# Performance work log

Measured on AMD Instinct MI355X. Metric: run time of the kernel, lower is better.

## Reference

```python
import jax, jax.numpy as jnp
import numpy as np

DIM = 256
NUM_HEADS = 8
HEAD_DIM = DIM // NUM_HEADS
CPB_HIDDEN = 512
B, N = 2, 2304
TABLE = 9025  # (2*48-1)**2


def _l2norm(t, eps=1e-12):
    # matches torch F.normalize(dim=-1): x / max(||x||, eps)
    n = jnp.sqrt(jnp.sum(t * t, axis=-1, keepdims=True))
    return t / jnp.maximum(n, eps)


def setup_inputs() -> dict:
    key = jax.random.key(0)
    ks = jax.random.split(key, 12)
    x = jax.random.normal(ks[0], (B, N, DIM), dtype=jnp.float32)
    relative_pos_index = jax.random.randint(ks[1], (N, N), 0, TABLE, dtype=jnp.int64)
    relative_coords_table = jax.random.uniform(ks[2], (TABLE, 2), dtype=jnp.float32) * 2.0 - 1.0
    seq_length_scale = jnp.ones((1,), dtype=jnp.float32) * jnp.log2(jnp.float32(N))
    padding_mask = jnp.zeros((B, N), dtype=jnp.int32)
    s = 0.02
    W_qkv = jax.random.normal(ks[3], (3 * DIM, DIM), dtype=jnp.float32) * s
    b_qkv = jnp.zeros((3 * DIM,), dtype=jnp.float32)
    # temperature init: log(exp(1/0.24) - 1) so softplus(temperature) = 1/0.24
    temperature = jnp.full((NUM_HEADS, 1, 1), float(np.log(np.expm1(1.0 / 0.24))), dtype=jnp.float32)
    query_embedding = jax.random.normal(ks[4], (NUM_HEADS, 1, HEAD_DIM), dtype=jnp.float32) * s
    W_proj = jax.random.normal(ks[5], (DIM, DIM), dtype=jnp.float32) * s
    b_proj = jnp.zeros((DIM,), dtype=jnp.float32)
    W_cpb1 = jax.random.normal(ks[6], (CPB_HIDDEN, 2), dtype=jnp.float32) * s
    b_cpb1 = jnp.zeros((CPB_HIDDEN,), dtype=jnp.float32)
    W_cpb2 = jax.random.normal(ks[7], (NUM_HEADS, CPB_HIDDEN), dtype=jnp.float32) * s
    b_cpb2 = jnp.zeros((NUM_HEADS,), dtype=jnp.float32)
    return {
        'x': x, 'relative_pos_index': relative_pos_index,
        'relative_coords_table': relative_coords_table,
        'seq_length_scale': seq_length_scale, 'padding_mask': padding_mask,
        'W_qkv': W_qkv, 'b_qkv': b_qkv, 'temperature': temperature,
        'query_embedding': query_embedding, 'W_proj': W_proj, 'b_proj': b_proj,
        'W_cpb1': W_cpb1, 'b_cpb1': b_cpb1, 'W_cpb2': W_cpb2, 'b_cpb2': b_cpb2,
    }


def reference(x, relative_pos_index, relative_coords_table, seq_length_scale,
              padding_mask, W_qkv, b_qkv, temperature, query_embedding,
              W_proj, b_proj, W_cpb1, b_cpb1, W_cpb2, b_cpb2):
    Bx, Nx, C = x.shape
    h, d = NUM_HEADS, HEAD_DIM
    # qkv projection -> (B, 3h, N, d); first h heads = q, then k, then v
    qkv = (jnp.einsum('bnc,oc->bno', x, W_qkv) + b_qkv)
    qkv = qkv.reshape(Bx, Nx, 3 * h, d).transpose(0, 2, 1, 3)
    q, k, v = qkv[:, :h], qkv[:, h:2 * h], qkv[:, 2 * h:]
    # CPB relative bias: (T,2) -> (T,h) -> (h,N,N) via gather
    hid = jax.nn.relu(relative_coords_table @ W_cpb1.T + b_cpb1)
    tab = hid @ W_cpb2.T + b_cpb2                    # (T, h)
    rel_bias = tab.T[:, relative_pos_index.reshape(-1)].reshape(h, Nx, Nx)
    # cosine-sim attention with learned query embedding + softplus temperature
    scale = jax.nn.softplus(temperature) * seq_length_scale[0]   # (h,1,1)
    qn = (_l2norm(q) + query_embedding) * scale                  # (B,h,N,d)
    kn = _l2norm(k)
    attn = jnp.einsum('bhnd,bhmd->bhnm', qn, kn) + rel_bias
    attn = jax.nn.softmax(attn, axis=-1)
    out = jnp.einsum('bhnm,bhmd->bhnd', attn, v)
    out = out.transpose(0, 2, 1, 3).reshape(Bx, Nx, C)
    out = out @ W_proj.T + b_proj
    return out
```

## Files before the change

### kernel.cpp

```cpp
#include <hip/hip_runtime.h>
#include <math.h>

#define DIMC 256
#define NHEADS 8
#define HDIM 32
#define CPBH 512
#define BB 2
#define NSEQ 2304
#define TAB 9025
#define TABP 9040
#define RTOT (BB*NHEADS*NSEQ)
#define SPLITS 4
#define MSP (NSEQ/SPLITS)
#define PBS 36
#define NCHUNK (NSEQ/32)
#define LOG2E 1.44269504088896340736f

#define IDXP_ELEMS    (NSEQ * NCHUNK * 16)
#define IDXP4_BLOCKS  (IDXP_ELEMS / 1024)
#define CPB_BLOCKS    ((TAB + 63) / 64)
#define QKV_BLOCKS    (12 * 72)

typedef unsigned short ushort;
typedef __attribute__((ext_vector_type(8))) short short8;
typedef __attribute__((ext_vector_type(4))) short short4v;
typedef __attribute__((ext_vector_type(4))) float f32x4;

#define MFMA16(a,b,c) __builtin_amdgcn_mfma_f32_16x16x32_bf16((a),(b),(c),0,0,0)

#define GL16(SRC, DST) __builtin_amdgcn_global_load_lds( \
    (const __attribute__((address_space(1))) void*)(SRC), \
    (__attribute__((address_space(3))) void*)(DST), 16, 0, 0)

__device__ __forceinline__ ushort f2bf(float x) {
  unsigned u = __float_as_uint(x);
  u += 0x7FFFu + ((u >> 16) & 1u);
  return (ushort)(u >> 16);
}
__device__ __forceinline__ float bf2f(ushort b) {
  return __uint_as_float(((unsigned)b) << 16);
}
__device__ __forceinline__ float fexp2(float x) {
#if defined(__has_builtin)
#if __has_builtin(__builtin_amdgcn_exp2f)
  return __builtin_amdgcn_exp2f(x);
#else
  return exp2f(x);
#endif
#else
  return exp2f(x);
#endif
}
__device__ __forceinline__ unsigned pack_trunc(float p0, float p1) {
  return __builtin_amdgcn_perm(__float_as_uint(p1), __float_as_uint(p0), 0x07060302u);
}
__device__ __forceinline__ void cvt8(const float* __restrict__ p, short8* hi, short8* lo) {
  float4 v0 = *(const float4*)p;
  float4 v1 = *(const float4*)(p + 4);
  float vv[8] = {v0.x, v0.y, v0.z, v0.w, v1.x, v1.y, v1.z, v1.w};
  short8 h, l;
#pragma unroll
  for (int i = 0; i < 8; ++i) {
    ushort hh = f2bf(vv[i]);
    h[i] = (short)hh;
    l[i] = (short)f2bf(vv[i] - bf2f(hh));
  }
  *hi = h; *lo = l;
}

__launch_bounds__(256)
__global__ void pack_kernel(const int* __restrict__ idx, unsigned* __restrict__ idxP) {
  int t4 = blockIdx.x * 256 + threadIdx.x;
  int grp = t4 >> 4;
  int ch = grp % NCHUNK;
  int n4 = grp / NCHUNK;
  int m = ch * 32 + (t4 & 15);
  unsigned o[4];
#pragma unroll
  for (int i = 0; i < 4; ++i) {
    unsigned lo = (unsigned)idx[(size_t)(n4 * 4 + i) * NSEQ + m];
    unsigned hi = (unsigned)idx[(size_t)(n4 * 4 + i) * NSEQ + m + 16];
    o[i] = lo | (hi << 16);
  }
  *(uint4*)&idxP[(size_t)t4 * 4] = *(const uint4*)o;
}

__launch_bounds__(256)
__global__ void pre_kernel(const float* __restrict__ x, const float* __restrict__ wq,
                           const float* __restrict__ tbl, const float* __restrict__ W1,
                           const float* __restrict__ b1, const float* __restrict__ W2,
                           const float* __restrict__ b2,
                           const float* __restrict__ bias, const float* __restrict__ temp,
                           const float* __restrict__ sls, const float* __restrict__ qe,
                           ushort* __restrict__ qhi, ushort* __restrict__ qlo,
                           ushort* __restrict__ khi, ushort* __restrict__ klo,
                           ushort* __restrict__ vT, ushort* __restrict__ tabBf) {
  __shared__ __align__(16) ushort smemu[33792];
  int blk = blockIdx.x;
  int tid = threadIdx.x;

  if (blk < CPB_BLOCKS) {
    float* smem = (float*)smemu;
    float* w1b = smem;
    float* w2t = smem + 2048;
    float* part = smem + 6144;
    for (int i = tid; i < CPBH; i += 256) {
      w1b[i * 4 + 0] = W1[2 * i];
      w1b[i * 4 + 1] = W1[2 * i + 1];
      w1b[i * 4 + 2] = b1[i];
      w1b[i * 4 + 3] = 0.f;
    }
    for (int i = tid; i < CPBH * NHEADS; i += 256)
      w2t[(i & (CPBH - 1)) * NHEADS + (i >> 9)] = W2[i];
    int tl = tid & 63, jc = tid >> 6;
    int t = blk * 64 + tl;
    bool valid = t < TAB;
    float c0 = 0.f, c1 = 0.f;
    if (valid) { c0 = tbl[2 * t]; c1 = tbl[2 * t + 1]; }
    __syncthreads();
    float acc[NHEADS];
#pragma unroll
    for (int h = 0; h < NHEADS; ++h) acc[h] = 0.f;
    for (int j = jc * 128; j < jc * 128 + 128; ++j) {
      float4 wv = *(const float4*)&w1b[j * 4];
      float hid = fmaxf(fmaf(c0, wv.x, fmaf(c1, wv.y, wv.z)), 0.f);
      float4 wa = *(const float4*)&w2t[j * NHEADS];
      float4 wb = *(const float4*)&w2t[j * NHEADS + 4];
      acc[0] = fmaf(hid, wa.x, acc[0]);
      acc[1] = fmaf(hid, wa.y, acc[1]);
      acc[2] = fmaf(hid, wa.z, acc[2]);
      acc[3] = fmaf(hid, wa.w, acc[3]);
      acc[4] = fmaf(hid, wb.x, acc[4]);
      acc[5] = fmaf(hid, wb.y, acc[5]);
      acc[6] = fmaf(hid, wb.z, acc[6]);
      acc[7] = fmaf(hid, wb.w, acc[7]);
    }
#pragma unroll
    for (int h = 0; h < NHEADS; ++h) part[((size_t)jc * 64 + tl) * NHEADS + h] = acc[h];
    __syncthreads();
    if (jc == 0 && valid) {
#pragma unroll
      for (int h = 0; h < NHEADS; ++h) {
        float s = b2[h];
#pragma unroll
        for (int p = 0; p < 4; ++p) s += part[((size_t)p * 64 + tl) * NHEADS + h];
        tabBf[h * TABP + t] = f2bf(s * LOG2E);
      }
    }
  } else {
    ushort* bsh = smemu;
    ushort* bsl = smemu + 64 * 264;
    float (*vbuf)[65] = (float(*)[65])smemu;
    int t = blk - CPB_BLOCKS;
    int n0 = (t % 12) * 64, m0 = (t / 12) * 64;
    int lane = tid & 63, w = tid >> 6;
    int g = lane >> 4, c = lane & 15;
    int mw = m0 + w * 16;
    const int K = DIMC;

    {
      int rr = tid >> 2, cq = (tid & 3) * 64;
#pragma unroll
      for (int j = 0; j < 64; j += 8) {
        short8 hh, ll;
        cvt8(&wq[(size_t)(n0 + rr) * K + cq + j], &hh, &ll);
        *(short8*)&bsh[rr * 264 + cq + j] = hh;
        *(short8*)&bsl[rr * 264 + cq + j] = ll;
      }
    }
    __syncthreads();

    f32x4 acc[4] = {{0,0,0,0},{0,0,0,0},{0,0,0,0},{0,0,0,0}};
#pragma unroll 2
    for (int k0 = 0; k0 < K; k0 += 32) {
      short8 ah, al;
      cvt8(&x[(size_t)(mw + c) * K + k0 + g * 8], &ah, &al);
#pragma unroll
      for (int nt = 0; nt < 4; ++nt) {
        int br = (nt * 16 + c) * 264 + k0 + g * 8;
        short8 bh = *(const short8*)&bsh[br];
        short8 bl = *(const short8*)&bsl[br];
        acc[nt] = MFMA16(ah, bh, acc[nt]);
        acc[nt] = MFMA16(al, bh, acc[nt]);
        acc[nt] = MFMA16(ah, bl, acc[nt]);
      }
    }
#pragma unroll
    for (int nt = 0; nt < 4; ++nt) {
      float bv = bias[n0 + nt * 16 + c];
#pragma unroll
      for (int r = 0; r < 4; ++r) acc[nt][r] += bv;
    }
    __syncthreads();

    int b = (m0 >= NSEQ) ? 1 : 0;
    int nb = m0 - b * NSEQ;
    int sect = n0 >> 8;
    int hloc = (n0 & 255) >> 5;

    if (sect < 2) {
#pragma unroll
      for (int H = 0; H < 2; ++H) {
        int head = hloc + H;
        float scale = (sect == 0) ? log1pf(expf(temp[head])) * sls[0] * LOG2E : 0.f;
#pragma unroll
        for (int r = 0; r < 4; ++r) {
          float ss = acc[2*H][r]*acc[2*H][r] + acc[2*H+1][r]*acc[2*H+1][r];
          ss += __shfl_xor(ss, 1);
          ss += __shfl_xor(ss, 2);
          ss += __shfl_xor(ss, 4);
          ss += __shfl_xor(ss, 8);
          float inv = 1.f / fmaxf(sqrtf(ss), 1e-12f);
#pragma unroll
          for (int half = 0; half < 2; ++half) {
            int d = half * 16 + c;
            float val = acc[2*H + half][r] * inv;
            if (sect == 0) val = (val + qe[head * HDIM + d]) * scale;
            vbuf[w * 16 + g * 4 + r][H * 32 + d] = val;
          }
        }
      }
      __syncthreads();
      int plane = tid >> 7;
      int seg = tid & 127;
      int head = seg >> 6, row = seg & 63;
      const float* srcrow = &vbuf[row][head * 32];
      ushort out16[32];
#pragma unroll
      for (int i = 0; i < 32; ++i) {
        float v = srcrow[i];
        ushort hh = f2bf(v);
        out16[i] = plane ? f2bf(v - bf2f(hh)) : hh;
      }
      ushort* dstp = plane ? (sect == 0 ? qlo : klo) : (sect == 0 ? qhi : khi);
      size_t off = ((size_t)(b * NHEADS + hloc + head) * NSEQ + nb + row) * HDIM;
#pragma unroll
      for (int q4 = 0; q4 < 4; ++q4)
        *(int4*)&dstp[off + q4 * 8] = ((int4*)out16)[q4];
    } else {
#pragma unroll
      for (int nt = 0; nt < 4; ++nt)
#pragma unroll
        for (int r = 0; r < 4; ++r)
          vbuf[w * 16 + g * 4 + r][nt * 16 + c] = acc[nt][r];
      __syncthreads();
      int hbase = (n0 - 512) >> 5;
#pragma unroll
      for (int it = 0; it < 16; ++it) {
        int dloc = (tid >> 6) * 16 + it;
        int p = tid & 63;
        int pp = p & 31;
        int nsrc = (p & 32) + (pp & 1) * 16 + (pp >> 1);
        float v = vbuf[nsrc][dloc];
        int head = hbase + (dloc >> 5), d = dloc & 31;
        vT[((size_t)((b * NHEADS + head) * HDIM + d)) * NSEQ + nb + p] = f2bf(v);
      }
    }
  }
}

__launch_bounds__(256)
__global__ void attn_kernel(const ushort* __restrict__ qhi, const ushort* __restrict__ qlo,
                            const ushort* __restrict__ khi, const ushort* __restrict__ klo,
                            const ushort* __restrict__ vT, const ushort* __restrict__ tabBf,
                            const unsigned* __restrict__ idxP,
                            float* __restrict__ pO, float* __restrict__ pL) {
  __shared__ ushort tbf[10240];
  __shared__ __align__(16) ushort pbuf[16][16 * PBS];
  __shared__ __align__(16) ushort stg[2][6144];
  int tid = threadIdx.x;
  int lane = tid & 63;
  int w = tid >> 6;

  int bid = blockIdx.x;
  int qb = bid >> 5;
  int k8 = bid & 7;
  int j4 = (bid >> 3) & 3;
  int y  = k8 + 8 * j4;
  int s = y & 3, h = y >> 2;

  const ushort* tsrc = tabBf + h * TABP;
#pragma unroll
  for (int i = 0; i < 5; ++i) {
    int off = i * 2048 + tid * 8;
    *(int4*)&tbf[off] = *(const int4*)&tsrc[off];
  }

  int g = lane >> 4, c = lane & 15;
  int q0 = qb * 128 + w * 32;
  int qg0 = q0 >> 2;
  size_t rowA = (size_t)h * NSEQ;
  size_t rowB = (size_t)(NHEADS + h) * NSEQ;
  int m0 = s * MSP;

  int su   = tid & 127;
  int srow = su & 31;
  int sslt = su >> 5;
  const ushort* kb0 = (tid < 128) ? khi : klo;
  const ushort* sA = kb0 + (rowA + m0 + srow) * HDIM + sslt * 8;
  const ushort* sB = kb0 + (rowB + m0 + srow) * HDIM + sslt * 8;
  const ushort* sV = vT + ((size_t)(((tid < 128) ? h : NHEADS + h) * HDIM + srow)) * NSEQ
                     + m0 + sslt * 8;
  unsigned dwb = (unsigned)(tid & 192) * 8;

#define STAGE(DP) do {                         \
    GL16(sA, (DP) + dwb);                      \
    GL16(sB, (DP) + 2048 + dwb);               \
    GL16(sV, (DP) + 4096 + dwb);               \
    sA += 32 * HDIM; sB += 32 * HDIM; sV += 32; \
  } while (0)

  short8 qA0h = *(const short8*)&qhi[(rowA + q0 + c) * HDIM + g * 8];
  short8 qA0l = *(const short8*)&qlo[(rowA + q0 + c) * HDIM + g * 8];
  short8 qA1h = *(const short8*)&qhi[(rowA + q0 + 16 + c) * HDIM + g * 8];
  short8 qA1l = *(const short8*)&qlo[(rowA + q0 + 16 + c) * HDIM + g * 8];
  short8 qB0h = *(const short8*)&qhi[(rowB + q0 + c) * HDIM + g * 8];
  short8 qB0l = *(const short8*)&qlo[(rowB + q0 + c) * HDIM + g * 8];
  short8 qB1h = *(const short8*)&qhi[(rowB + q0 + 16 + c) * HDIM + g * 8];
  short8 qB1l = *(const short8*)&qlo[(rowB + q0 + 16 + c) * HDIM + g * 8];

  const unsigned IOFF1 = 4u * NCHUNK * 64;
  unsigned oIb = (unsigned)(((unsigned)(qg0 + g) * NCHUNK + (m0 >> 5)) * 64 + c * 4);
  unsigned oI  = oIb;
  uint4 ia = *(const uint4*)&idxP[oI];
  uint4 ja = *(const uint4*)&idxP[oI + IOFF1];

  STAGE(&stg[0][0]);
  __syncthreads();

  short one = (c == 0) ? (short)0x3F80 : (short)0;
  short8 onesB = {one, one, one, one, one, one, one, one};

  f32x4 oa00 = {0,0,0,0}, oa01 = {0,0,0,0}, oa10 = {0,0,0,0}, oa11 = {0,0,0,0};
  f32x4 ob00 = {0,0,0,0}, ob01 = {0,0,0,0}, ob10 = {0,0,0,0}, ob11 = {0,0,0,0};
  f32x4 la0 = {0,0,0,0}, la1 = {0,0,0,0}, lb0 = {0,0,0,0}, lb1 = {0,0,0,0};
  ushort* pba0 = pbuf[w * 4];
  ushort* pba1 = pbuf[w * 4 + 1];
  ushort* pbb0 = pbuf[w * 4 + 2];
  ushort* pbb1 = pbuf[w * 4 + 3];

  int kbo = g * 256 + c * 8;
  int cur = 0;

  for (int mt = m0; mt < m0 + MSP; mt += 32) {
    bool lastit = (mt + 32 >= m0 + MSP);

    asm volatile("s_waitcnt vmcnt(0)" ::: "memory");
    __builtin_amdgcn_s_barrier();
    __builtin_amdgcn_sched_barrier(0);

    unsigned oIn = lastit ? oIb : oI + 64;
    uint4 ian = *(const uint4*)&idxP[oIn];
    uint4 jan = *(const uint4*)&idxP[oIn + IOFF1];
    oI = oIn;
    if (!lastit) STAGE(&stg[cur ^ 1][0]);

    const ushort* S = &stg[cur][0];
    short8 ak0h = *(const short8*)&S[kbo];
    short8 ak1h = *(const short8*)&S[kbo + 128];
    short8 ak0l = *(const short8*)&S[1024 + kbo];
    short8 ak1l = *(const short8*)&S[1024 + kbo + 128];
    short8 bk0h = *(const short8*)&S[2048 + kbo];
    short8 bk1h = *(const short8*)&S[2048 + kbo + 128];
    short8 bk0l = *(const short8*)&S[3072 + kbo];
    short8 bk1l = *(const short8*)&S[3072 + kbo + 128];

    f32x4 sa0 = {0,0,0,0}, sa1 = {0,0,0,0}, ta0 = {0,0,0,0}, ta1 = {0,0,0,0};
    f32x4 sb0 = {0,0,0,0}, sb1 = {0,0,0,0}, tb0 = {0,0,0,0}, tb1 = {0,0,0,0};
    sa0 = MFMA16(qA0h, ak0h, sa0);
    sa1 = MFMA16(qA0h, ak1h, sa1);
    ta0 = MFMA16(qA1h, ak0h, ta0);
    ta1 = MFMA16(qA1h, ak1h, ta1);
    sb0 = MFMA16(qB0h, bk0h, sb0);
    sb1 = MFMA16(qB0h, bk1h, sb1);
    tb0 = MFMA16(qB1h, bk0h, tb0);
    tb1 = MFMA16(qB1h, bk1h, tb1);
    sa0 = MFMA16(qA0l, ak0h, sa0);
    sa1 = MFMA16(qA0l, ak1h, sa1);
    ta0 = MFMA16(qA1l, ak0h, ta0);
    ta1 = MFMA16(qA1l, ak1h, ta1);
    sb0 = MFMA16(qB0l, bk0h, sb0);
    sb1 = MFMA16(qB0l, bk1h, sb1);
    tb0 = MFMA16(qB1l, bk0h, tb0);
    tb1 = MFMA16(qB1l, bk1h, tb1);
    sa0 = MFMA16(qA0h, ak0l, sa0);
    sa1 = MFMA16(qA0h, ak1l, sa1);
    ta0 = MFMA16(qA1h, ak0l, ta0);
    ta1 = MFMA16(qA1h, ak1l, ta1);
    sb0 = MFMA16(qB0h, bk0l, sb0);
    sb1 = MFMA16(qB0h, bk1l, sb1);
    tb0 = MFMA16(qB1h, bk0l, tb0);
    tb1 = MFMA16(qB1h, bk1l, tb1);

    unsigned ip[4] = {ia.x, ia.y, ia.z, ia.w};
    unsigned jp[4] = {ja.x, ja.y, ja.z, ja.w};
#pragma unroll
    for (int r = 0; r < 4; ++r) {
      float b0 = bf2f(tbf[ip[r] & 0xFFFF]);
      float b1 = bf2f(tbf[ip[r] >> 16]);
      *(unsigned*)&pba0[(g * 4 + r) * PBS + 2 * c] =
          pack_trunc(fexp2(sa0[r] + b0), fexp2(sa1[r] + b1));
      *(unsigned*)&pbb0[(g * 4 + r) * PBS + 2 * c] =
          pack_trunc(fexp2(sb0[r] + b0), fexp2(sb1[r] + b1));
      float d0 = bf2f(tbf[jp[r] & 0xFFFF]);
      float d1 = bf2f(tbf[jp[r] >> 16]);
      *(unsigned*)&pba1[(g * 4 + r) * PBS + 2 * c] =
          pack_trunc(fexp2(ta0[r] + d0), fexp2(ta1[r] + d1));
      *(unsigned*)&pbb1[(g * 4 + r) * PBS + 2 * c] =
          pack_trunc(fexp2(tb0[r] + d0), fexp2(tb1[r] + d1));
    }

#define LOADP(PB, DST) do {                                             \
    short4v pA_ = *(const short4v*)&(PB)[c * PBS + g * 8];              \
    short4v pB_ = *(const short4v*)&(PB)[c * PBS + g * 8 + 4];          \
    DST = __builtin_shufflevector(pA_, pB_, 0, 1, 2, 3, 4, 5, 6, 7);    \
  } while (0)
    short8 pfa0, pfa1, pfb0, pfb1;
    LOADP(pba0, pfa0);
    LOADP(pba1, pfa1);
    LOADP(pbb0, pfb0);
    LOADP(pbb1, pfb1);
#undef LOADP

    short8 vf0 = *(const short8*)&S[4096 + kbo];
    short8 vf1 = *(const short8*)&S[4096 + kbo + 128];
    short8 wf0 = *(const short8*)&S[5120 + kbo];
    short8 wf1 = *(const short8*)&S[5120 + kbo + 128];

    oa00 = MFMA16(pfa0, vf0, oa00);
    oa01 = MFMA16(pfa0, vf1, oa01);
    oa10 = MFMA16(pfa1, vf0, oa10);
    oa11 = MFMA16(pfa1, vf1, oa11);
    ob00 = MFMA16(pfb0, wf0, ob00);
    ob01 = MFMA16(pfb0, wf1, ob01);
    ob10 = MFMA16(pfb1, wf0, ob10);
    ob11 = MFMA16(pfb1, wf1, ob11);
    la0  = MFMA16(pfa0, onesB, la0);
    la1  = MFMA16(pfa1, onesB, la1);
    lb0  = MFMA16(pfb0, onesB, lb0);
    lb1  = MFMA16(pfb1, onesB, lb1);

    ia = ian; ja = jan;
    cur ^= 1;
  }
#undef STAGE

  asm volatile("s_waitcnt vmcnt(0)" ::: "memory");

  size_t prowA = (size_t)s * RTOT + rowA;
  size_t prowB = (size_t)s * RTOT + rowB;
#pragma unroll
  for (int r = 0; r < 4; ++r) {
    size_t pa0 = prowA + q0 + g * 4 + r;
    pO[pa0 * HDIM + c]      = oa00[r];
    pO[pa0 * HDIM + 16 + c] = oa01[r];
    size_t pa1 = pa0 + 16;
    pO[pa1 * HDIM + c]      = oa10[r];
    pO[pa1 * HDIM + 16 + c] = oa11[r];
    size_t pb0 = prowB + q0 + g * 4 + r;
    pO[pb0 * HDIM + c]      = ob00[r];
    pO[pb0 * HDIM + 16 + c] = ob01[r];
    size_t pb1 = pb0 + 16;
    pO[pb1 * HDIM + c]      = ob10[r];
    pO[pb1 * HDIM + 16 + c] = ob11[r];
    if (c == 0) {
      pL[pa0] = la0[r]; pL[pa1] = la1[r];
      pL[pb0] = lb0[r]; pL[pb1] = lb1[r];
    }
  }
}

#define ALD 264
__launch_bounds__(256)
__global__ void gemm_proj_fused(const float* __restrict__ pO, const float* __restrict__ pL,
                                const float* __restrict__ Wp,
                                const float* __restrict__ bias, float* __restrict__ C) {
  __shared__ __align__(16) ushort Ahs[32 * ALD];
  __shared__ __align__(16) ushort Als[32 * ALD];
  int tid = threadIdx.x;
  int m0 = blockIdx.x * 32;
  int b = (m0 >= NSEQ) ? 1 : 0;
  int nb = m0 - b * NSEQ;

  {
    int rr = tid >> 3;
    int q  = tid & 3;
    int hp = (tid >> 2) & 1;
    int n = nb + rr;
#pragma unroll
    for (int hh = 0; hh < 4; ++hh) {
      int h = hp * 4 + hh;
      size_t bhn = (size_t)(b * NHEADS + h) * NSEQ + n;
      float L = 0.f;
#pragma unroll
      for (int sp = 0; sp < SPLITS; ++sp) L += pL[(size_t)sp * RTOT + bhn];
      float inv = 1.f / L;
      float a[8] = {0.f, 0.f, 0.f, 0.f, 0.f, 0.f, 0.f, 0.f};
#pragma unroll
      for (int sp = 0; sp < SPLITS; ++sp) {
        const float* src = &pO[((size_t)sp * RTOT + bhn) * HDIM + q * 8];
        float4 v0 = *(const float4*)&src[0];
        float4 v1 = *(const float4*)&src[4];
        a[0] += v0.x; a[1] += v0.y; a[2] += v0.z; a[3] += v0.w;
        a[4] += v1.x; a[5] += v1.y; a[6] += v1.z; a[7] += v1.w;
      }
      ushort hi8[8], lo8[8];
#pragma unroll
      for (int i = 0; i < 8; ++i) {
        float v = a[i] * inv;
        ushort hh2 = f2bf(v);
        hi8[i] = hh2;
        lo8[i] = f2bf(v - bf2f(hh2));
      }
      int k = h * 32 + q * 8;
      *(int4*)&Ahs[rr * ALD + k] = *(int4*)hi8;
      *(int4*)&Als[rr * ALD + k] = *(int4*)lo8;
    }
  }
  __syncthreads();

  int lane = tid & 63, w = tid >> 6;
  int g = lane >> 4, c = lane & 15;
  int n0 = w * 64;
  f32x4 acc[2][4] = {};
  for (int k0 = 0; k0 < DIMC; k0 += 32) {
    short8 bfh[4], bfl[4];
#pragma unroll
    for (int nt = 0; nt < 4; ++nt)
      cvt8(&Wp[(size_t)(n0 + nt * 16 + c) * DIMC + k0 + g * 8], &bfh[nt], &bfl[nt]);
#pragma unroll
    for (int mt = 0; mt < 2; ++mt) {
      short8 ah = *(const short8*)&Ahs[(mt * 16 + c) * ALD + k0 + g * 8];
      short8 al = *(const short8*)&Als[(mt * 16 + c) * ALD + k0 + g * 8];
#pragma unroll
      for (int nt = 0; nt < 4; ++nt) {
        acc[mt][nt] = MFMA16(ah, bfh[nt], acc[mt][nt]);
        acc[mt][nt] = MFMA16(al, bfh[nt], acc[mt][nt]);
        acc[mt][nt] = MFMA16(ah, bfl[nt], acc[mt][nt]);
      }
    }
  }
#pragma unroll
  for (int nt = 0; nt < 4; ++nt) {
    float bv = bias[n0 + nt * 16 + c];
#pragma unroll
    for (int mt = 0; mt < 2; ++mt)
#pragma unroll
      for (int r = 0; r < 4; ++r)
        C[(size_t)(m0 + mt * 16 + g * 4 + r) * DIMC + n0 + nt * 16 + c] = acc[mt][nt][r] + bv;
  }
}

extern "C" void kernel_launch(void* const* d_in, const int* in_sizes, int n_in,
                              void* d_out, int out_size, void* d_ws, size_t ws_size,
                              hipStream_t stream) {
  const float* x    = (const float*)d_in[0];
  const int*   idx  = (const int*)d_in[1];
  const float* tbl  = (const float*)d_in[2];
  const float* sls  = (const float*)d_in[3];
  const float* Wqkv = (const float*)d_in[5];
  const float* bqkv = (const float*)d_in[6];
  const float* temp = (const float*)d_in[7];
  const float* qe   = (const float*)d_in[8];
  const float* Wp   = (const float*)d_in[9];
  const float* bp   = (const float*)d_in[10];
  const float* W1   = (const float*)d_in[11];
  const float* b1   = (const float*)d_in[12];
  const float* W2   = (const float*)d_in[13];
  const float* b2   = (const float*)d_in[14];

  float* ws   = (float*)d_ws;
  float* pO   = ws;
  float* pL   = pO + (size_t)SPLITS * RTOT * HDIM;
  unsigned* idxP = (unsigned*)(pL + (size_t)SPLITS * RTOT);
  ushort* u   = (ushort*)(idxP + IDXP_ELEMS);
  ushort* qhi = u;                u += (size_t)RTOT * HDIM;
  ushort* qlo = u;                u += (size_t)RTOT * HDIM;
  ushort* khi = u;                u += (size_t)RTOT * HDIM;
  ushort* klo = u;                u += (size_t)RTOT * HDIM;
  ushort* vT  = u;                u += (size_t)RTOT * HDIM;
  ushort* tabBf = u;              u += 73728;
  float* out  = (float*)d_out;

  pack_kernel<<<dim3(IDXP4_BLOCKS), dim3(256), 0, stream>>>(idx, idxP);
  pre_kernel<<<dim3(CPB_BLOCKS + QKV_BLOCKS), dim3(256), 0, stream>>>(
      x, Wqkv, tbl, W1, b1, W2, b2, bqkv, temp, sls, qe,
      qhi, qlo, khi, klo, vT, tabBf);
  attn_kernel<<<dim3((NSEQ / 128) * NHEADS * SPLITS), dim3(256), 0, stream>>>(
      qhi, qlo, khi, klo, vT, tabBf, idxP, pO, pL);
  gemm_proj_fused<<<dim3((BB * NSEQ) / 32), dim3(256), 0, stream>>>(
      pO, pL, Wp, bp, out);
}
```

Before: 197.8 us.

## Precompute bf16 hi/lo splits of x and weights once in pack kernel

Moves the fp32-to-bf16 hi/lo splitting of x, W_qkv and W_proj into the existing pack kernel as extra blocks that write the split arrays to workspace. The QKV GEMM and projection GEMM then load the pre-split bf16 data directly instead of converting repeatedly per tile. The projection GEMM is also retiled to 16 rows per block, doubling the grid for more parallelism. This adds an extra global write and read pass and more workspace memory in exchange for removing redundant conversions.

Measured after the change: 199.3 us. About the same (+0.7%).

```diff
diff --git a/kernel.cpp b/kernel.cpp
--- a/kernel.cpp
+++ b/kernel.cpp
@@ -18,6 +18,11 @@
 
 #define IDXP_ELEMS    (NSEQ * NCHUNK * 16)
 #define IDXP4_BLOCKS  (IDXP_ELEMS / 1024)
+#define XELEM   (BB*NSEQ*DIMC)
+#define WQELEM  (3*DIMC*DIMC)
+#define WPELEM  (DIMC*DIMC)
+#define CVT_THREADS ((XELEM + WQELEM + WPELEM) / 8)
+#define CVT_BLOCKS  (CVT_THREADS / 256)
 #define CPB_BLOCKS    ((TAB + 63) / 64)
 #define QKV_BLOCKS    (12 * 72)
 
@@ -69,24 +74,51 @@
 }
 
 __launch_bounds__(256)
-__global__ void pack_kernel(const int* __restrict__ idx, unsigned* __restrict__ idxP) {
-  int t4 = blockIdx.x * 256 + threadIdx.x;
-  int grp = t4 >> 4;
-  int ch = grp % NCHUNK;
-  int n4 = grp / NCHUNK;
-  int m = ch * 32 + (t4 & 15);
-  unsigned o[4];
-#pragma unroll
-  for (int i = 0; i < 4; ++i) {
-    unsigned lo = (unsigned)idx[(size_t)(n4 * 4 + i) * NSEQ + m];
-    unsigned hi = (unsigned)idx[(size_t)(n4 * 4 + i) * NSEQ + m + 16];
-    o[i] = lo | (hi << 16);
-  }
-  *(uint4*)&idxP[(size_t)t4 * 4] = *(const uint4*)o;
+__global__ void pack_kernel(const int* __restrict__ idx, unsigned* __restrict__ idxP,
+                            const float* __restrict__ x, const float* __restrict__ wq,
+                            const float* __restrict__ wp,
+                            ushort* __restrict__ xhi, ushort* __restrict__ xlo,
+                            ushort* __restrict__ wqhi, ushort* __restrict__ wqlo,
+                            ushort* __restrict__ wphi, ushort* __restrict__ wplo) {
+  int blk = blockIdx.x;
+  int tid = threadIdx.x;
+  if (blk < IDXP4_BLOCKS) {
+    int t4 = blk * 256 + tid;
+    int grp = t4 >> 4;
+    int ch = grp % NCHUNK;
+    int n4 = grp / NCHUNK;
+    int m = ch * 32 + (t4 & 15);
+    unsigned o[4];
+#pragma unroll
+    for (int i = 0; i < 4; ++i) {
+      unsigned lo = (unsigned)idx[(size_t)(n4 * 4 + i) * NSEQ + m];
+      unsigned hi = (unsigned)idx[(size_t)(n4 * 4 + i) * NSEQ + m + 16];
+      o[i] = lo | (hi << 16);
+    }
+    *(uint4*)&idxP[(size_t)t4 * 4] = *(const uint4*)o;
+  } else {
+    int t8 = (blk - IDXP4_BLOCKS) * 256 + tid;
+    const float* s;
+    ushort* dh;
+    ushort* dl;
+    int off;
+    if (t8 < XELEM / 8) {
+      s = x;  dh = xhi;  dl = xlo;  off = t8;
+    } else if (t8 < (XELEM + WQELEM) / 8) {
+      s = wq; dh = wqhi; dl = wqlo; off = t8 - XELEM / 8;
+    } else {
+      s = wp; dh = wphi; dl = wplo; off = t8 - (XELEM + WQELEM) / 8;
+    }
+    short8 hh, ll;
+    cvt8(&s[(size_t)off * 8], &hh, &ll);
+    *(short8*)&dh[(size_t)off * 8] = hh;
+    *(short8*)&dl[(size_t)off * 8] = ll;
+  }
 }
 
 __launch_bounds__(256)
-__global__ void pre_kernel(const float* __restrict__ x, const float* __restrict__ wq,
+__global__ void pre_kernel(const ushort* __restrict__ xhi, const ushort* __restrict__ xlo,
+                           const ushort* __restrict__ wqhi, const ushort* __restrict__ wqlo,
                            const float* __restrict__ tbl, const float* __restrict__ W1,
                            const float* __restrict__ b1, const float* __restrict__ W2,
                            const float* __restrict__ b2,
@@ -162,10 +194,10 @@
       int rr = tid >> 2, cq = (tid & 3) * 64;
 #pragma unroll
       for (int j = 0; j < 64; j += 8) {
-        short8 hh, ll;
-        cvt8(&wq[(size_t)(n0 + rr) * K + cq + j], &hh, &ll);
-        *(short8*)&bsh[rr * 264 + cq + j] = hh;
-        *(short8*)&bsl[rr * 264 + cq + j] = ll;
+        *(short8*)&bsh[rr * 264 + cq + j] =
+            *(const short8*)&wqhi[(size_t)(n0 + rr) * K + cq + j];
+        *(short8*)&bsl[rr * 264 + cq + j] =
+            *(const short8*)&wqlo[(size_t)(n0 + rr) * K + cq + j];
       }
     }
     __syncthreads();
@@ -173,8 +205,8 @@
     f32x4 acc[4] = {{0,0,0,0},{0,0,0,0},{0,0,0,0},{0,0,0,0}};
 #pragma unroll 2
     for (int k0 = 0; k0 < K; k0 += 32) {
-      short8 ah, al;
-      cvt8(&x[(size_t)(mw + c) * K + k0 + g * 8], &ah, &al);
+      short8 ah = *(const short8*)&xhi[(size_t)(mw + c) * K + k0 + g * 8];
+      short8 al = *(const short8*)&xlo[(size_t)(mw + c) * K + k0 + g * 8];
 #pragma unroll
       for (int nt = 0; nt < 4; ++nt) {
         int br = (nt * 16 + c) * 264 + k0 + g * 8;
@@ -473,81 +505,76 @@
 #define ALD 264
 __launch_bounds__(256)
 __global__ void gemm_proj_fused(const float* __restrict__ pO, const float* __restrict__ pL,
-                                const float* __restrict__ Wp,
+                                const ushort* __restrict__ wphi, const ushort* __restrict__ wplo,
                                 const float* __restrict__ bias, float* __restrict__ C) {
-  __shared__ __align__(16) ushort Ahs[32 * ALD];
-  __shared__ __align__(16) ushort Als[32 * ALD];
+  __shared__ __align__(16) ushort Ahs[16 * ALD];
+  __shared__ __align__(16) ushort Als[16 * ALD];
   int tid = threadIdx.x;
-  int m0 = blockIdx.x * 32;
+  int m0 = blockIdx.x * 16;
   int b = (m0 >= NSEQ) ? 1 : 0;
   int nb = m0 - b * NSEQ;
 
   {
-    int rr = tid >> 3;
-    int q  = tid & 3;
-    int hp = (tid >> 2) & 1;
-    int n = nb + rr;
-#pragma unroll
-    for (int hh = 0; hh < 4; ++hh) {
-      int h = hp * 4 + hh;
-      size_t bhn = (size_t)(b * NHEADS + h) * NSEQ + n;
-      float L = 0.f;
-#pragma unroll
-      for (int sp = 0; sp < SPLITS; ++sp) L += pL[(size_t)sp * RTOT + bhn];
-      float inv = 1.f / L;
-      float a[8] = {0.f, 0.f, 0.f, 0.f, 0.f, 0.f, 0.f, 0.f};
-#pragma unroll
-      for (int sp = 0; sp < SPLITS; ++sp) {
-        const float* src = &pO[((size_t)sp * RTOT + bhn) * HDIM + q * 8];
-        float4 v0 = *(const float4*)&src[0];
-        float4 v1 = *(const float4*)&src[4];
-        a[0] += v0.x; a[1] += v0.y; a[2] += v0.z; a[3] += v0.w;
-        a[4] += v1.x; a[5] += v1.y; a[6] += v1.z; a[7] += v1.w;
+    int row = tid >> 4;
+    int sub = tid & 15;
+    int hh2 = sub >> 1;
+    int half = sub & 1;
+    int n = nb + row;
+    size_t bhn = (size_t)(b * NHEADS + hh2) * NSEQ + n;
+    float L = 0.f;
+#pragma unroll
+    for (int sp = 0; sp < SPLITS; ++sp) L += pL[(size_t)sp * RTOT + bhn];
+    float inv = 1.f / L;
+    float a[16] = {0};
+#pragma unroll
+    for (int sp = 0; sp < SPLITS; ++sp) {
+      const float* src = &pO[((size_t)sp * RTOT + bhn) * HDIM + half * 16];
+#pragma unroll
+      for (int q = 0; q < 4; ++q) {
+        float4 v = *(const float4*)&src[q * 4];
+        a[q * 4 + 0] += v.x; a[q * 4 + 1] += v.y;
+        a[q * 4 + 2] += v.z; a[q * 4 + 3] += v.w;
       }
-      ushort hi8[8], lo8[8];
-#pragma unroll
-      for (int i = 0; i < 8; ++i) {
-        float v = a[i] * inv;
-        ushort hh2 = f2bf(v);
-        hi8[i] = hh2;
-        lo8[i] = f2bf(v - bf2f(hh2));
-      }
-      int k = h * 32 + q * 8;
-      *(int4*)&Ahs[rr * ALD + k] = *(int4*)hi8;
-      *(int4*)&Als[rr * ALD + k] = *(int4*)lo8;
-    }
+    }
+    ushort h16[16], l16[16];
+#pragma unroll
+    for (int i = 0; i < 16; ++i) {
+      float v = a[i] * inv;
+      ushort hh = f2bf(v);
+      h16[i] = hh;
+      l16[i] = f2bf(v - bf2f(hh));
+    }
+    int k = hh2 * 32 + half * 16;
+    *(int4*)&Ahs[row * ALD + k]     = ((int4*)h16)[0];
+    *(int4*)&Ahs[row * ALD + k + 8] = ((int4*)h16)[1];
+    *(int4*)&Als[row * ALD + k]     = ((int4*)l16)[0];
+    *(int4*)&Als[row * ALD + k + 8] = ((int4*)l16)[1];
   }
   __syncthreads();
 
   int lane = tid & 63, w = tid >> 6;
   int g = lane >> 4, c = lane & 15;
   int n0 = w * 64;
-  f32x4 acc[2][4] = {};
+  f32x4 acc[4] = {};
   for (int k0 = 0; k0 < DIMC; k0 += 32) {
-    short8 bfh[4], bfl[4];
-#pragma unroll
-    for (int nt = 0; nt < 4; ++nt)
-      cvt8(&Wp[(size_t)(n0 + nt * 16 + c) * DIMC + k0 + g * 8], &bfh[nt], &bfl[nt]);
-#pragma unroll
-    for (int mt = 0; mt < 2; ++mt) {
-      short8 ah = *(const short8*)&Ahs[(mt * 16 + c) * ALD + k0 + g * 8];
-      short8 al = *(const short8*)&Als[(mt * 16 + c) * ALD + k0 + g * 8];
-#pragma unroll
-      for (int nt = 0; nt < 4; ++nt) {
-        acc[mt][nt] = MFMA16(ah, bfh[nt], acc[mt][nt]);
-        acc[mt][nt] = MFMA16(al, bfh[nt], acc[mt][nt]);
-        acc[mt][nt] = MFMA16(ah, bfl[nt], acc[mt][nt]);
-      }
+    short8 ah = *(const short8*)&Ahs[c * ALD + k0 + g * 8];
+    short8 al = *(const short8*)&Als[c * ALD + k0 + g * 8];
+#pragma unroll
+    for (int nt = 0; nt < 4; ++nt) {
+      size_t wo = (size_t)(n0 + nt * 16 + c) * DIMC + k0 + g * 8;
+      short8 bh = *(const short8*)&wphi[wo];
+      short8 bl = *(const short8*)&wplo[wo];
+      acc[nt] = MFMA16(ah, bh, acc[nt]);
+      acc[nt] = MFMA16(al, bh, acc[nt]);
+      acc[nt] = MFMA16(ah, bl, acc[nt]);
     }
   }
 #pragma unroll
   for (int nt = 0; nt < 4; ++nt) {
     float bv = bias[n0 + nt * 16 + c];
 #pragma unroll
-    for (int mt = 0; mt < 2; ++mt)
-#pragma unroll
-      for (int r = 0; r < 4; ++r)
-        C[(size_t)(m0 + mt * 16 + g * 4 + r) * DIMC + n0 + nt * 16 + c] = acc[mt][nt][r] + bv;
+    for (int r = 0; r < 4; ++r)
+      C[(size_t)(m0 + g * 4 + r) * DIMC + n0 + nt * 16 + c] = acc[nt][r] + bv;
   }
 }
 
@@ -580,14 +607,21 @@
   ushort* klo = u;                u += (size_t)RTOT * HDIM;
   ushort* vT  = u;                u += (size_t)RTOT * HDIM;
   ushort* tabBf = u;              u += 73728;
+  ushort* xhi  = u;               u += XELEM;
+  ushort* xlo  = u;               u += XELEM;
+  ushort* wqhi = u;               u += WQELEM;
+  ushort* wqlo = u;               u += WQELEM;
+  ushort* wphi = u;               u += WPELEM;
+  ushort* wplo = u;               u += WPELEM;
   float* out  = (float*)d_out;
 
-  pack_kernel<<<dim3(IDXP4_BLOCKS), dim3(256), 0, stream>>>(idx, idxP);
+  pack_kernel<<<dim3(IDXP4_BLOCKS + CVT_BLOCKS), dim3(256), 0, stream>>>(
+      idx, idxP, x, Wqkv, Wp, xhi, xlo, wqhi, wqlo, wphi, wplo);
   pre_kernel<<<dim3(CPB_BLOCKS + QKV_BLOCKS), dim3(256), 0, stream>>>(
-      x, Wqkv, tbl, W1, b1, W2, b2, bqkv, temp, sls, qe,
+      xhi, xlo, wqhi, wqlo, tbl, W1, b1, W2, b2, bqkv, temp, sls, qe,
       qhi, qlo, khi, klo, vT, tabBf);
   attn_kernel<<<dim3((NSEQ / 128) * NHEADS * SPLITS), dim3(256), 0, stream>>>(
       qhi, qlo, khi, klo, vT, tabBf, idxP, pO, pL);
-  gemm_proj_fused<<<dim3((BB * NSEQ) / 32), dim3(256), 0, stream>>>(
-      pO, pL, Wp, bp, out);
-}
+  gemm_proj_fused<<<dim3((BB * NSEQ) / 16), dim3(256), 0, stream>>>(
+      pO, pL, wphi, wplo, bp, out);
+}
```
